# Performance work log

Hardware: AMD Instinct MI355X
Metric: run time of the kernel (lower is better)

## Reference

```python
import jax, jax.numpy as jnp
import numpy as np
from jax import lax

EPS = 1e-5

def _zpool(x):
    # cat(max over channel, mean over channel) -> [B,2,H,W]
    return jnp.concatenate([x.max(axis=1, keepdims=True), x.mean(axis=1, keepdims=True)], axis=1)

def _gate(x, w, g, b, m, v):
    # ZPool -> 7x7 conv (2->1, same pad) -> inference BN -> sigmoid -> scale input
    z = _zpool(x)
    y = lax.conv_general_dilated(z, w, (1, 1), [(3, 3), (3, 3)],
                                 dimension_numbers=('NCHW', 'OIHW', 'NCHW'))
    scale = g / jnp.sqrt(v + EPS)
    y = (y - m[None, :, None, None]) * scale[None, :, None, None] + b[None, :, None, None]
    return x * jax.nn.sigmoid(y)


def setup_inputs() -> dict:
    key = jax.random.key(0)
    ks = jax.random.split(key, 8)
    B, C, H, W = 8, 256, 64, 64
    inp = {
        'x': jax.random.normal(ks[0], (B, C, H, W), dtype=jnp.float32),
        'w_cw': jax.random.normal(ks[1], (1, 2, 7, 7), dtype=jnp.float32) * 0.1,
        'g_cw': jnp.ones((1,), jnp.float32), 'b_cw': jnp.zeros((1,), jnp.float32),
        'm_cw': jnp.zeros((1,), jnp.float32), 'v_cw': jnp.ones((1,), jnp.float32),
        'w_hc': jax.random.normal(ks[2], (1, 2, 7, 7), dtype=jnp.float32) * 0.1,
        'g_hc': jnp.ones((1,), jnp.float32), 'b_hc': jnp.zeros((1,), jnp.float32),
        'm_hc': jnp.zeros((1,), jnp.float32), 'v_hc': jnp.ones((1,), jnp.float32),
        'w_hw': jax.random.normal(ks[3], (1, 2, 7, 7), dtype=jnp.float32) * 0.1,
        'g_hw': jnp.ones((1,), jnp.float32), 'b_hw': jnp.zeros((1,), jnp.float32),
        'm_hw': jnp.zeros((1,), jnp.float32), 'v_hw': jnp.ones((1,), jnp.float32),
        'w1d': jax.random.normal(ks[4], (3, 1, 7), dtype=jnp.float32) * 0.1,
    }
    return inp


def reference(x, w_cw, g_cw, b_cw, m_cw, v_cw,
              w_hc, g_hc, b_hc, m_hc, v_hc,
              w_hw, g_hw, b_hw, m_hw, v_hw, w1d):
    # branch 1: attend over (C) with H as channel dim
    b1 = _gate(x.transpose(0, 2, 1, 3), w_cw, g_cw, b_cw, m_cw, v_cw).transpose(0, 2, 1, 3)
    # branch 2: attend with W as channel dim
    b2 = _gate(x.transpose(0, 3, 2, 1), w_hc, g_hc, b_hc, m_hc, v_hc).transpose(0, 3, 2, 1)
    # branch 3: spatial attention in native layout
    b3 = _gate(x, w_hw, g_hw, b_hw, m_hw, v_hw)

    x_out = (b1 + b2 + b3) / 3.0
    pooled = x_out.mean(axis=(2, 3))                     # [B, C]
    logits = lax.conv_general_dilated(pooled[:, None, :], w1d, (1,), [(3, 3)],
                                      dimension_numbers=('NCH', 'OIH', 'NCH'))  # [B,3,C]
    wts = jax.nn.softmax(logits, axis=1)[..., None, None]  # [B,3,C,1,1]
    branches = jnp.stack([b1, b2, b3], axis=1)             # [B,3,C,H,W]
    return (wts * branches).sum(axis=1)
```

## Files before the change

### kernel.cpp

```cpp
#include <hip/hip_runtime.h>
#include <math.h>

#define BB 8
#define CC 256
#define HH 64
#define WW 64
#define EPS 1e-5f
#define PSCALE (1.f / 12288.f)

__global__ __launch_bounds__(256) void pool_kernel(
    const float* __restrict__ x,
    float* __restrict__ z1max, float* __restrict__ z1mean,
    float* __restrict__ z2tmax, float* __restrict__ z2tmean,
    float* __restrict__ z3max, float* __restrict__ z3mean,
    float* __restrict__ pooled)
{
    __shared__ float smem[HH * 65 + 512];
    int blk = blockIdx.x;
    int t = threadIdx.x;

    if (blk < 8) pooled[blk * 256 + t] = 0.f;

    if (blk < BB * CC) {
        int bc = blk;
        const float4* xt4 = (const float4*)x + (size_t)bc * 1024;
        float* tile = smem;
        float* red  = smem + HH * 65;

        #pragma unroll
        for (int i = 0; i < 4; ++i) {
            int idx = t + i * 256;
            float4 v = xt4[idx];
            int h = idx >> 4, w0 = (idx & 15) * 4;
            float* d = &tile[h * 65 + w0];
            d[0] = v.x; d[1] = v.y; d[2] = v.z; d[3] = v.w;
        }
        __syncthreads();

        {
            int w = t & 63, hg = t >> 6;
            float m = -INFINITY, s = 0.f;
            #pragma unroll
            for (int i = 0; i < 16; ++i) {
                float v = tile[(hg * 16 + i) * 65 + w];
                m = fmaxf(m, v); s += v;
            }
            red[t] = m; red[256 + t] = s;
        }
        __syncthreads();
        if (t < 64) {
            float m = red[t], s = red[256 + t];
            #pragma unroll
            for (int g = 1; g < 4; ++g) { m = fmaxf(m, red[g * 64 + t]); s += red[256 + g * 64 + t]; }
            z1max [bc * WW + t] = m;
            z1mean[bc * WW + t] = s * (1.f / 64.f);
        }
        __syncthreads();

        {
            int h = t & 63, wg = t >> 6;
            float m = -INFINITY, s = 0.f;
            #pragma unroll
            for (int i = 0; i < 16; ++i) {
                float v = tile[h * 65 + wg * 16 + i];
                m = fmaxf(m, v); s += v;
            }
            red[t] = m; red[256 + t] = s;
        }
        __syncthreads();
        if (t < 64) {
            float m = red[t], s = red[256 + t];
            #pragma unroll
            for (int g = 1; g < 4; ++g) { m = fmaxf(m, red[g * 64 + t]); s += red[256 + g * 64 + t]; }
            z2tmax [bc * HH + t] = m;
            z2tmean[bc * HH + t] = s * (1.f / 64.f);
        }
    } else {
        int bh = blk - BB * CC;
        int b = bh >> 6, h = bh & 63;
        int wq = t & 15, cgp = t >> 4;

        const float4* base = (const float4*)x
            + ((size_t)b * CC * HH * WW + (size_t)h * WW) / 4 + wq;
        float4 m = make_float4(-INFINITY, -INFINITY, -INFINITY, -INFINITY);
        float4 s = make_float4(0.f, 0.f, 0.f, 0.f);
        #pragma unroll 4
        for (int i = 0; i < 16; ++i) {
            float4 v = base[(size_t)(cgp * 16 + i) * 1024];
            m.x = fmaxf(m.x, v.x); m.y = fmaxf(m.y, v.y);
            m.z = fmaxf(m.z, v.z); m.w = fmaxf(m.w, v.w);
            s.x += v.x; s.y += v.y; s.z += v.z; s.w += v.w;
        }
        float4* mred = (float4*)smem;
        float4* sred = (float4*)smem + 256;
        mred[t] = m; sred[t] = s;
        __syncthreads();
        if (t < 16) {
            float4 mm = mred[t], ss = sred[t];
            #pragma unroll
            for (int g = 1; g < 16; ++g) {
                float4 mv = mred[g * 16 + t], sv = sred[g * 16 + t];
                mm.x = fmaxf(mm.x, mv.x); mm.y = fmaxf(mm.y, mv.y);
                mm.z = fmaxf(mm.z, mv.z); mm.w = fmaxf(mm.w, mv.w);
                ss.x += sv.x; ss.y += sv.y; ss.z += sv.z; ss.w += sv.w;
            }
            ss.x *= (1.f / 256.f); ss.y *= (1.f / 256.f);
            ss.z *= (1.f / 256.f); ss.w *= (1.f / 256.f);
            *(float4*)(z3max  + bh * WW + t * 4) = mm;
            *(float4*)(z3mean + bh * WW + t * 4) = ss;
        }
    }
}

#define TROWS 38
#define TPITCH 70
#define TELEMS (TROWS * TPITCH)

__global__ __launch_bounds__(256) void gate_kernel(
    const float* __restrict__ x,
    const float* __restrict__ z1max, const float* __restrict__ z1mean,
    const float* __restrict__ w0p, const float* g0, const float* b0,
    const float* m0, const float* v0, float* __restrict__ s1,
    const float* __restrict__ z2tmax, const float* __restrict__ z2tmean,
    const float* __restrict__ w1p, const float* g1, const float* b1,
    const float* m1, const float* v1, float* __restrict__ s2,
    const float* __restrict__ z3max, const float* __restrict__ z3mean,
    const float* __restrict__ w2p, const float* g2, const float* b2,
    const float* m2, const float* v2, float* __restrict__ s3,
    float* __restrict__ pooled)
{
    __shared__ float sm[2 * TELEMS + 100];
    int blk = blockIdx.x;
    int t = threadIdx.x;

    if (blk < 128) {
        const int br  = blk >> 6;
        const int sub = blk & 63;
        const int b   = sub >> 3;
        const int rt  = (sub & 7) * 32;
        const float* zm = br ? z2tmax  : z1max;
        const float* za = br ? z2tmean : z1mean;
        const float* wp = br ? w1p : w0p;
        const float* gp = br ? g1 : g0;  const float* bp = br ? b1 : b0;
        const float* mp = br ? m1 : m0;  const float* vp = br ? v1 : v0;
        float* sout = br ? s2 : s1;

        float* tm  = sm;
        float* ta  = sm + TELEMS;
        float* wsm = sm + 2 * TELEMS;

        if (t < 98) {
            int p = (t >= 49) ? 1 : 0;
            int q = t - p * 49;
            wsm[t] = wp[p * 49 + (br ? (q % 7) * 7 + q / 7 : q)];
        }
        for (int idx = t; idx < TELEMS; idx += 256) {
            int r  = idx / TPITCH;
            int cc = idx - r * TPITCH;
            int grow = rt + r - 3, gcol = cc - 3;
            bool ok = (grow >= 0) & (grow < 256) & (gcol >= 0) & (gcol < 64);
            size_t gi = ((size_t)b * 256 + grow) * 64 + gcol;
            tm[idx] = ok ? zm[gi] : 0.f;
            ta[idx] = ok ? za[gi] : 0.f;
        }
        __syncthreads();

        const int col = t & 63, rg = t >> 6;
        const int lo0 = rg * 8;

        float acc[8];
        #pragma unroll
        for (int o = 0; o < 8; ++o) acc[o] = 0.f;

        #pragma unroll
        for (int rl = 0; rl < 14; ++rl) {
            const float* rowm = &tm[(lo0 + rl) * TPITCH + col];
            const float* rowa = &ta[(lo0 + rl) * TPITCH + col];
            #pragma unroll
            for (int dc = 0; dc < 7; ++dc) {
                float vmax = rowm[dc], vmean = rowa[dc];
                #pragma unroll
                for (int o = 0; o < 8; ++o) {
                    int dr = rl - o;
                    if (dr >= 0 && dr < 7) {
                        acc[o] = fmaf(wsm[dr * 7 + dc],      vmax,  acc[o]);
                        acc[o] = fmaf(wsm[49 + dr * 7 + dc], vmean, acc[o]);
                    }
                }
            }
        }

        const float bnscale = gp[0] * rsqrtf(vp[0] + EPS);
        const float bnmean = mp[0], bnbias = bp[0];
        #pragma unroll
        for (int o = 0; o < 8; ++o) {
            int lo = lo0 + o;
            float y = (acc[o] - bnmean) * bnscale + bnbias;
            float sv = 1.f / (1.f + __expf(-y));
            sout[((size_t)b * 256 + rt + lo) * 64 + col] = sv;
            float prod = sv * ta[(lo + 3) * TPITCH + col + 3];
            #pragma unroll
            for (int off = 32; off >= 1; off >>= 1) prod += __shfl_down(prod, off);
            if ((t & 63) == 0) atomicAdd(&pooled[b * 256 + rt + lo], 64.f * prod);
        }
    } else {
        float* t3m   = sm;
        float* t3a   = sm + 7 * TPITCH;
        float* w2sm  = sm + 14 * TPITCH;
        float* s3row = sm + 14 * TPITCH + 98;

        int bh = blk - 128;
        int b = bh >> 6, h = bh & 63;

        if (t < 98) w2sm[t] = w2p[t];
        for (int idx = t; idx < 7 * TPITCH; idx += 256) {
            int r  = idx / TPITCH;
            int cc = idx - r * TPITCH;
            int grow = h + r - 3, gcol = cc - 3;
            bool ok = (grow >= 0) & (grow < 64) & (gcol >= 0) & (gcol < 64);
            size_t gi = ((size_t)b * 64 + grow) * 64 + gcol;
            t3m[idx] = ok ? z3max[gi]  : 0.f;
            t3a[idx] = ok ? z3mean[gi] : 0.f;
        }
        __syncthreads();

        if (t < 64) {
            float acc = 0.f;
            #pragma unroll
            for (int dr = 0; dr < 7; ++dr) {
                #pragma unroll
                for (int dc = 0; dc < 7; ++dc) {
                    acc = fmaf(w2sm[dr * 7 + dc],      t3m[dr * TPITCH + t + dc], acc);
                    acc = fmaf(w2sm[49 + dr * 7 + dc], t3a[dr * TPITCH + t + dc], acc);
                }
            }
            float scale = g2[0] * rsqrtf(v2[0] + EPS);
            float y = (acc - m2[0]) * scale + b2[0];
            float v = 1.f / (1.f + __expf(-y));
            s3[bh * WW + t] = v;
            s3row[t] = v;
        }
        __syncthreads();

        int wv = t >> 6, l = t & 63;
        int c_local = l >> 2, wsub = l & 3;
        const float4* s3q4 = (const float4*)s3row;

        float4 xv[16];
        #pragma unroll
        for (int pass = 0; pass < 4; ++pass) {
            int c = pass * 64 + (wv << 4) + c_local;
            const float4* xr4 = (const float4*)x
                + ((size_t)(b * 256 + c) * 4096 + h * 64) / 4 + wsub * 4;
            #pragma unroll
            for (int j = 0; j < 4; ++j) xv[pass * 4 + j] = xr4[j];
        }
        #pragma unroll
        for (int pass = 0; pass < 4; ++pass) {
            int c = pass * 64 + (wv << 4) + c_local;
            float acc = 0.f;
            #pragma unroll
            for (int j = 0; j < 4; ++j) {
                float4 a = xv[pass * 4 + j];
                float4 sv = s3q4[wsub * 4 + j];
                acc += a.x * sv.x + a.y * sv.y + a.z * sv.z + a.w * sv.w;
            }
            acc += __shfl_xor(acc, 1);
            acc += __shfl_xor(acc, 2);
            if (wsub == 0) atomicAdd(&pooled[b * 256 + c], acc);
        }
    }
}

__global__ __launch_bounds__(256) void final_kernel(
    const float* __restrict__ x,
    const float* __restrict__ s1, const float* __restrict__ s2,
    const float* __restrict__ s3, const float* __restrict__ pooled,
    const float* __restrict__ w1d, float* __restrict__ out)
{
    __shared__ float kk[3];
    int t = threadIdx.x;
    int i4 = blockIdx.x * 256 + t;
    int rest = i4 >> 4;
    int h = rest & 63;
    int c = (rest >> 6) & 255;
    int b = rest >> 14;

    if (t == 0) {
        float lg0 = 0.f, lg1 = 0.f, lg2 = 0.f;
        #pragma unroll
        for (int jj = 0; jj < 7; ++jj) {
            int cc2 = c + jj - 3;
            float pv = (cc2 >= 0 && cc2 < CC) ? pooled[b * CC + cc2] : 0.f;
            lg0 += w1d[jj] * pv;
            lg1 += w1d[7 + jj] * pv;
            lg2 += w1d[14 + jj] * pv;
        }
        lg0 *= PSCALE; lg1 *= PSCALE; lg2 *= PSCALE;
        float mx = fmaxf(lg0, fmaxf(lg1, lg2));
        float e0 = __expf(lg0 - mx), e1 = __expf(lg1 - mx), e2 = __expf(lg2 - mx);
        float inv = 1.f / (e0 + e1 + e2);
        kk[0] = e0 * inv; kk[1] = e1 * inv; kk[2] = e2 * inv;
    }
    __syncthreads();
    float k0 = kk[0], k1 = kk[1], k2 = kk[2];

    int w0 = (i4 & 15) * 4;
    const float4 x4  = *(const float4*)(x  + (size_t)i4 * 4);
    const float4 s1v = *(const float4*)(s1 + ((size_t)(b * CC + c)) * WW + w0);
    const float  s2v = s2[rest];
    const float4 s3v = *(const float4*)(s3 + ((size_t)(b * HH + h)) * WW + w0);

    float4 o;
    o.x = x4.x * (k0 * s1v.x + k1 * s2v + k2 * s3v.x);
    o.y = x4.y * (k0 * s1v.y + k1 * s2v + k2 * s3v.y);
    o.z = x4.z * (k0 * s1v.z + k1 * s2v + k2 * s3v.z);
    o.w = x4.w * (k0 * s1v.w + k1 * s2v + k2 * s3v.w);
    *(float4*)(out + (size_t)i4 * 4) = o;
}

extern "C" void kernel_launch(void* const* d_in, const int* in_sizes, int n_in,
                              void* d_out, int out_size, void* d_ws, size_t ws_size,
                              hipStream_t stream)
{
    const float* x    = (const float*)d_in[0];
    const float* w_cw = (const float*)d_in[1];
    const float* g_cw = (const float*)d_in[2];
    const float* b_cw = (const float*)d_in[3];
    const float* m_cw = (const float*)d_in[4];
    const float* v_cw = (const float*)d_in[5];
    const float* w_hc = (const float*)d_in[6];
    const float* g_hc = (const float*)d_in[7];
    const float* b_hc = (const float*)d_in[8];
    const float* m_hc = (const float*)d_in[9];
    const float* v_hc = (const float*)d_in[10];
    const float* w_hw = (const float*)d_in[11];
    const float* g_hw = (const float*)d_in[12];
    const float* b_hw = (const float*)d_in[13];
    const float* m_hw = (const float*)d_in[14];
    const float* v_hw = (const float*)d_in[15];
    const float* w1d  = (const float*)d_in[16];
    float* out = (float*)d_out;

    float* ws = (float*)d_ws;
    const size_t N1 = (size_t)BB * CC * WW;
    const size_t N2 = (size_t)BB * CC * HH;
    const size_t N3 = (size_t)BB * HH * WW;
    float* z1max   = ws;
    float* z1mean  = z1max   + N1;
    float* z2tmax  = z1mean  + N1;
    float* z2tmean = z2tmax  + N2;
    float* z3max   = z2tmean + N2;
    float* z3mean  = z3max   + N3;
    float* s1      = z3mean  + N3;
    float* s2      = s1 + N1;
    float* s3      = s2 + N2;
    float* pooled  = s3 + N3;

    pool_kernel<<<BB * CC + BB * HH, 256, 0, stream>>>(
        x, z1max, z1mean, z2tmax, z2tmean, z3max, z3mean, pooled);

    gate_kernel<<<128 + BB * HH, 256, 0, stream>>>(
        x,
        z1max, z1mean, w_cw, g_cw, b_cw, m_cw, v_cw, s1,
        z2tmax, z2tmean, w_hc, g_hc, b_hc, m_hc, v_hc, s2,
        z3max, z3mean, w_hw, g_hw, b_hw, m_hw, v_hw, s3,
        pooled);

    final_kernel<<<(BB * CC * HH * WW / 4) / 256, 256, 0, stream>>>(
        x, s1, s2, s3, pooled, w1d, out);
}
```

Measured before the change: 141.9 us.

## Replace smem tile transpose in pool kernel with shuffles; split gate branch-3 blocks

The per-(b,c) pooling path drops the padded shared-memory tile and its multiple barriers. Row reductions now use wave shuffles over the float4 lanes, and column reductions use register accumulation plus one small shared-memory reduce, which cuts LDS traffic and shrinks the LDS footprint to allow higher occupancy. In the gate kernel, the spatial branch is split into four blocks per (b,h), each covering 64 channels. This gives more parallelism and fewer registers per thread, but each block recomputes the 7x7 conv and repeats the staging of the z3 halo.

```diff
diff --git a/kernel.cpp b/kernel.cpp
--- a/kernel.cpp
+++ b/kernel.cpp
@@ -15,7 +15,7 @@
     float* __restrict__ z3max, float* __restrict__ z3mean,
     float* __restrict__ pooled)
 {
-    __shared__ float smem[HH * 65 + 512];
+    __shared__ float4 sm4[512];
     int blk = blockIdx.x;
     int t = threadIdx.x;
 
@@ -24,56 +24,55 @@
     if (blk < BB * CC) {
         int bc = blk;
         const float4* xt4 = (const float4*)x + (size_t)bc * 1024;
-        float* tile = smem;
-        float* red  = smem + HH * 65;
-
+        const int wq = t & 15, hb = t >> 4;
+
+        float4 v0 = xt4[(hb     ) * 16 + wq];
+        float4 v1 = xt4[(hb + 16) * 16 + wq];
+        float4 v2 = xt4[(hb + 32) * 16 + wq];
+        float4 v3 = xt4[(hb + 48) * 16 + wq];
+
+        float4 vv[4] = {v0, v1, v2, v3};
         #pragma unroll
         for (int i = 0; i < 4; ++i) {
-            int idx = t + i * 256;
-            float4 v = xt4[idx];
-            int h = idx >> 4, w0 = (idx & 15) * 4;
-            float* d = &tile[h * 65 + w0];
-            d[0] = v.x; d[1] = v.y; d[2] = v.z; d[3] = v.w;
-        }
-        __syncthreads();
-
-        {
-            int w = t & 63, hg = t >> 6;
-            float m = -INFINITY, s = 0.f;
-            #pragma unroll
-            for (int i = 0; i < 16; ++i) {
-                float v = tile[(hg * 16 + i) * 65 + w];
-                m = fmaxf(m, v); s += v;
-            }
-            red[t] = m; red[256 + t] = s;
-        }
-        __syncthreads();
-        if (t < 64) {
-            float m = red[t], s = red[256 + t];
-            #pragma unroll
-            for (int g = 1; g < 4; ++g) { m = fmaxf(m, red[g * 64 + t]); s += red[256 + g * 64 + t]; }
-            z1max [bc * WW + t] = m;
-            z1mean[bc * WW + t] = s * (1.f / 64.f);
-        }
-        __syncthreads();
-
-        {
-            int h = t & 63, wg = t >> 6;
-            float m = -INFINITY, s = 0.f;
-            #pragma unroll
-            for (int i = 0; i < 16; ++i) {
-                float v = tile[h * 65 + wg * 16 + i];
-                m = fmaxf(m, v); s += v;
-            }
-            red[t] = m; red[256 + t] = s;
-        }
-        __syncthreads();
-        if (t < 64) {
-            float m = red[t], s = red[256 + t];
-            #pragma unroll
-            for (int g = 1; g < 4; ++g) { m = fmaxf(m, red[g * 64 + t]); s += red[256 + g * 64 + t]; }
-            z2tmax [bc * HH + t] = m;
-            z2tmean[bc * HH + t] = s * (1.f / 64.f);
+            float4 u = vv[i];
+            float hm = fmaxf(fmaxf(u.x, u.y), fmaxf(u.z, u.w));
+            float hs = (u.x + u.y) + (u.z + u.w);
+            #pragma unroll
+            for (int off = 1; off < 16; off <<= 1) {
+                hm = fmaxf(hm, __shfl_xor(hm, off));
+                hs += __shfl_xor(hs, off);
+            }
+            if (wq == 0) {
+                int h = hb + i * 16;
+                z2tmax [bc * HH + h] = hm;
+                z2tmean[bc * HH + h] = hs * (1.f / 64.f);
+            }
+        }
+
+        float4 m4, s4;
+        m4.x = fmaxf(fmaxf(v0.x, v1.x), fmaxf(v2.x, v3.x));
+        m4.y = fmaxf(fmaxf(v0.y, v1.y), fmaxf(v2.y, v3.y));
+        m4.z = fmaxf(fmaxf(v0.z, v1.z), fmaxf(v2.z, v3.z));
+        m4.w = fmaxf(fmaxf(v0.w, v1.w), fmaxf(v2.w, v3.w));
+        s4.x = (v0.x + v1.x) + (v2.x + v3.x);
+        s4.y = (v0.y + v1.y) + (v2.y + v3.y);
+        s4.z = (v0.z + v1.z) + (v2.z + v3.z);
+        s4.w = (v0.w + v1.w) + (v2.w + v3.w);
+        sm4[t] = m4; sm4[256 + t] = s4;
+        __syncthreads();
+        if (t < 16) {
+            float4 m = sm4[t], s = sm4[256 + t];
+            #pragma unroll
+            for (int g = 1; g < 16; ++g) {
+                float4 a = sm4[g * 16 + t], b2 = sm4[256 + g * 16 + t];
+                m.x = fmaxf(m.x, a.x); m.y = fmaxf(m.y, a.y);
+                m.z = fmaxf(m.z, a.z); m.w = fmaxf(m.w, a.w);
+                s.x += b2.x; s.y += b2.y; s.z += b2.z; s.w += b2.w;
+            }
+            s.x *= (1.f / 64.f); s.y *= (1.f / 64.f);
+            s.z *= (1.f / 64.f); s.w *= (1.f / 64.f);
+            *(float4*)(z1max  + bc * WW + t * 4) = m;
+            *(float4*)(z1mean + bc * WW + t * 4) = s;
         }
     } else {
         int bh = blk - BB * CC;
@@ -91,8 +90,8 @@
             m.z = fmaxf(m.z, v.z); m.w = fmaxf(m.w, v.w);
             s.x += v.x; s.y += v.y; s.z += v.z; s.w += v.w;
         }
-        float4* mred = (float4*)smem;
-        float4* sred = (float4*)smem + 256;
+        float4* mred = sm4;
+        float4* sred = sm4 + 256;
         mred[t] = m; sred[t] = s;
         __syncthreads();
         if (t < 16) {
@@ -115,6 +114,7 @@
 #define TROWS 38
 #define TPITCH 70
 #define TELEMS (TROWS * TPITCH)
+#define SMEMF (2 * TELEMS + 100)
 
 __global__ __launch_bounds__(256) void gate_kernel(
     const float* __restrict__ x,
@@ -129,7 +129,7 @@
     const float* m2, const float* v2, float* __restrict__ s3,
     float* __restrict__ pooled)
 {
-    __shared__ float sm[2 * TELEMS + 100];
+    __shared__ float sm[SMEMF];
     int blk = blockIdx.x;
     int t = threadIdx.x;
 
@@ -204,16 +204,16 @@
             if ((t & 63) == 0) atomicAdd(&pooled[b * 256 + rt + lo], 64.f * prod);
         }
     } else {
+        int u = blk - 128;
+        int cq = u & 3, h = (u >> 2) & 63, b = u >> 8;
+
         float* t3m   = sm;
-        float* t3a   = sm + 7 * TPITCH;
-        float* w2sm  = sm + 14 * TPITCH;
-        float* s3row = sm + 14 * TPITCH + 98;
-
-        int bh = blk - 128;
-        int b = bh >> 6, h = bh & 63;
+        float* t3a   = sm + 490;
+        float* w2sm  = sm + 980;
+        float* s3row = sm + 1080;
 
         if (t < 98) w2sm[t] = w2p[t];
-        for (int idx = t; idx < 7 * TPITCH; idx += 256) {
+        for (int idx = t; idx < 490; idx += 256) {
             int r  = idx / TPITCH;
             int cc = idx - r * TPITCH;
             int grow = h + r - 3, gcol = cc - 3;
@@ -237,38 +237,26 @@
             float scale = g2[0] * rsqrtf(v2[0] + EPS);
             float y = (acc - m2[0]) * scale + b2[0];
             float v = 1.f / (1.f + __expf(-y));
-            s3[bh * WW + t] = v;
             s3row[t] = v;
-        }
-        __syncthreads();
-
-        int wv = t >> 6, l = t & 63;
-        int c_local = l >> 2, wsub = l & 3;
+            if (cq == 0) s3[((b << 6) + h) * 64 + t] = v;
+        }
+        __syncthreads();
+
+        int c_local = t >> 2, wsub = t & 3;
+        int c = cq * 64 + c_local;
+        const float4* xr4 = (const float4*)x
+            + ((size_t)(b * 256 + c) * 4096 + h * 64) / 4 + wsub * 4;
         const float4* s3q4 = (const float4*)s3row;
-
-        float4 xv[16];
-        #pragma unroll
-        for (int pass = 0; pass < 4; ++pass) {
-            int c = pass * 64 + (wv << 4) + c_local;
-            const float4* xr4 = (const float4*)x
-                + ((size_t)(b * 256 + c) * 4096 + h * 64) / 4 + wsub * 4;
-            #pragma unroll
-            for (int j = 0; j < 4; ++j) xv[pass * 4 + j] = xr4[j];
-        }
-        #pragma unroll
-        for (int pass = 0; pass < 4; ++pass) {
-            int c = pass * 64 + (wv << 4) + c_local;
-            float acc = 0.f;
-            #pragma unroll
-            for (int j = 0; j < 4; ++j) {
-                float4 a = xv[pass * 4 + j];
-                float4 sv = s3q4[wsub * 4 + j];
-                acc += a.x * sv.x + a.y * sv.y + a.z * sv.z + a.w * sv.w;
-            }
-            acc += __shfl_xor(acc, 1);
-            acc += __shfl_xor(acc, 2);
-            if (wsub == 0) atomicAdd(&pooled[b * 256 + c], acc);
-        }
+        float acc = 0.f;
+        #pragma unroll
+        for (int j = 0; j < 4; ++j) {
+            float4 a = xr4[j];
+            float4 sv = s3q4[wsub * 4 + j];
+            acc += a.x * sv.x + a.y * sv.y + a.z * sv.z + a.w * sv.w;
+        }
+        acc += __shfl_xor(acc, 1);
+        acc += __shfl_xor(acc, 2);
+        if (wsub == 0) atomicAdd(&pooled[b * 256 + c], acc);
     }
 }
 
@@ -360,7 +348,7 @@
     pool_kernel<<<BB * CC + BB * HH, 256, 0, stream>>>(
         x, z1max, z1mean, z2tmax, z2tmean, z3max, z3mean, pooled);
 
-    gate_kernel<<<128 + BB * HH, 256, 0, stream>>>(
+    gate_kernel<<<128 + 2048, 256, 0, stream>>>(
         x,
         z1max, z1mean, w_cw, g_cw, b_cw, m_cw, v_cw, s1,
         z2tmax, z2tmean, w_hc, g_hc, b_hc, m_hc, v_hc, s2,
```

Result: slower. 151.0 us (+6.5%).
